# Kernel optimization log

Measured on AMD Instinct MI355X. Metric: run time of the kernel, lower is better.

Reference implementation:

```python
import jax, jax.numpy as jnp
import numpy as np

EPS = 1e-6


def _phi(x):
    # feature map: ELU(x) + 1, strictly positive
    return jax.nn.elu(x) + 1.0


def setup_inputs() -> dict:
    key = jax.random.key(0)
    kq, kk, kv, km, kz = jax.random.split(key, 5)
    B, H, T, D = 2, 32, 4096, 128
    Q = jax.random.normal(kq, (B, H, T, D), dtype=jnp.float32)
    K = jax.random.normal(kk, (B, H, T, D), dtype=jnp.float32)
    V = jax.random.normal(kv, (B, H, T, D), dtype=jnp.float32)
    M = jax.random.normal(km, (H, D, D), dtype=jnp.float32)
    z = jax.random.uniform(kz, (H, D), dtype=jnp.float32)
    return {"Q": Q, "K": K, "V": V, "M": M, "z": z}


def reference(Q, K, V, M, z):
    # ---- retrieve(Q) ----
    phi_Q = _phi(Q)                                   # (b,h,t,d)
    retrieved = jnp.einsum('bhtd,hde->bhte', phi_Q, M)
    norm = jnp.einsum('bhtd,hd->bht', phi_Q, z)[..., None]
    out = retrieved / jnp.maximum(norm, EPS)          # (b,h,t,d)

    # ---- update(K, V): detached (stop_gradient) running accumulation ----
    phi_K_b = _phi(jax.lax.stop_gradient(K)).mean(0)  # (h,t,d)
    V_b = jax.lax.stop_gradient(V).mean(0)            # (h,t,d)
    M_new = M + jnp.einsum('htd,hte->hde', phi_K_b, V_b)
    z_new = z + phi_K_b.sum(1)
    return out, M_new, z_new
```

## Files before the change

kernel.cpp:

```cpp
#include <hip/hip_runtime.h>
#include <cstdint>
#include <cstddef>


typedef __bf16 bf16x8 __attribute__((ext_vector_type(8)));
typedef float  f32x4  __attribute__((ext_vector_type(4)));
typedef unsigned short us4v __attribute__((ext_vector_type(4)));
typedef unsigned short us8v __attribute__((ext_vector_type(8)));

#define NB 2
#define NH 32
#define NT 4096
#define ND 128
#define NC 16
#define TCH (NT / NC)
#define EPSF 1e-6f

__device__ __forceinline__ float phi_f(float x) {
    return x > 0.0f ? x + 1.0f : __expf(x);
}

__device__ __forceinline__ unsigned short f2bf(float f) {
    union { float f; unsigned u; } c; c.f = f;
    unsigned r = c.u + 0x7FFFu + ((c.u >> 16) & 1u);
    return (unsigned short)(r >> 16);
}

__global__ __launch_bounds__(256) void k_prep(const float* __restrict__ M,
                                              unsigned short* __restrict__ Mt) {
    int idx = blockIdx.x * 256 + threadIdx.x;
    int h = idx >> 14, rem = idx & 16383;
    int e = rem >> 7, d = rem & 127;
    Mt[idx] = f2bf(M[(h << 14) + (d << 7) + e]);
}

__global__ __launch_bounds__(256) void k_out(const float* __restrict__ Q,
                                             const unsigned short* __restrict__ Mt,
                                             const float* __restrict__ z,
                                             float* __restrict__ out) {
    __shared__ unsigned short As[128 * 136];
    __shared__ unsigned short Bs[128 * 136];
    __shared__ float nrm[128];

    const int tid  = threadIdx.x;
    const int tile = blockIdx.x & 31;
    const int bh   = blockIdx.x >> 5;
    const int h    = bh & 31;
    const float* Qb = Q + ((size_t)bh * NT + (size_t)tile * 128) * ND;

    {
        const us8v* src = (const us8v*)(Mt + (size_t)h * 128 * 128);
#pragma unroll
        for (int i = 0; i < 8; ++i) {
            int idx = i * 256 + tid;
            int e  = idx >> 4;
            int d8 = (idx & 15) << 3;
            us8v v = src[idx];
            *(us8v*)&Bs[e * 136 + d8] = v;
        }
    }
    {
        const int d0 = (tid & 31) << 2;
        const int rb = tid >> 5;
        const float4 zv = *(const float4*)(z + h * ND + d0);
#pragma unroll
        for (int i = 0; i < 16; ++i) {
            int r = rb + i * 8;
            float4 q = *(const float4*)(Qb + (size_t)r * ND + d0);
            float p0 = phi_f(q.x), p1 = phi_f(q.y), p2 = phi_f(q.z), p3 = phi_f(q.w);
            float part = p0 * zv.x + p1 * zv.y + p2 * zv.z + p3 * zv.w;
            part += __shfl_xor(part, 1);
            part += __shfl_xor(part, 2);
            part += __shfl_xor(part, 4);
            part += __shfl_xor(part, 8);
            part += __shfl_xor(part, 16);
            if ((tid & 31) == 0) nrm[r] = part;
            us4v pk;
            pk.x = f2bf(p0); pk.y = f2bf(p1); pk.z = f2bf(p2); pk.w = f2bf(p3);
            *(us4v*)&As[r * 136 + d0] = pk;
        }
    }
    __syncthreads();

    const int lane = tid & 63, wave = tid >> 6;
    const int mw = (wave & 1) << 6, nw = (wave >> 1) << 6;
    const int l15 = lane & 15, qd = lane >> 4;

    f32x4 acc[4][4];
#pragma unroll
    for (int a = 0; a < 4; ++a)
#pragma unroll
        for (int b = 0; b < 4; ++b) acc[a][b] = (f32x4){0.f, 0.f, 0.f, 0.f};

#pragma unroll
    for (int kk = 0; kk < 4; ++kk) {
        const int k0 = kk * 32 + qd * 8;
        bf16x8 af[4], bfv[4];
#pragma unroll
        for (int im = 0; im < 4; ++im)
            af[im] = *(const bf16x8*)&As[(mw + im * 16 + l15) * 136 + k0];
#pragma unroll
        for (int in = 0; in < 4; ++in)
            bfv[in] = *(const bf16x8*)&Bs[(nw + in * 16 + l15) * 136 + k0];
#pragma unroll
        for (int im = 0; im < 4; ++im)
#pragma unroll
            for (int in = 0; in < 4; ++in)
                acc[im][in] = __builtin_amdgcn_mfma_f32_16x16x32_bf16(
                    af[im], bfv[in], acc[im][in], 0, 0, 0);
    }

    float inv[4][4];
#pragma unroll
    for (int im = 0; im < 4; ++im)
#pragma unroll
        for (int rg = 0; rg < 4; ++rg)
            inv[im][rg] = 1.0f / fmaxf(nrm[mw + im * 16 + qd * 4 + rg], EPSF);

    float* outb = out + ((size_t)bh * NT + (size_t)tile * 128) * ND;
#pragma unroll
    for (int im = 0; im < 4; ++im)
#pragma unroll
        for (int in = 0; in < 4; ++in) {
            int col = nw + in * 16 + l15;
#pragma unroll
            for (int rg = 0; rg < 4; ++rg) {
                int row = mw + im * 16 + qd * 4 + rg;
                outb[(size_t)row * ND + col] = acc[im][in][rg] * inv[im][rg];
            }
        }
}

__global__ __launch_bounds__(256) void k_upd(const float* __restrict__ K,
                                             const float* __restrict__ V,
                                             float* __restrict__ part,
                                             float* __restrict__ zpart) {
    __shared__ unsigned short Kl[128 * 72];
    __shared__ unsigned short Vl[128 * 72];
    __shared__ float zacc[128];

    const int tid = threadIdx.x;
    const int h   = blockIdx.x >> 4;
    const int ch  = blockIdx.x & 15;
    const size_t bstr = (size_t)NH * NT * ND;
    const float* K0 = K + (size_t)h * NT * ND + (size_t)ch * TCH * ND;
    const float* K1 = K0 + bstr;
    const float* V0 = V + (size_t)h * NT * ND + (size_t)ch * TCH * ND;
    const float* V1 = V0 + bstr;
    if (tid < 128) zacc[tid] = 0.0f;

    const int d0 = (tid & 31) << 2;
    const int tb = tid >> 5;
    const int lane = tid & 63, wave = tid >> 6;
    const int mw = (wave & 1) << 6, nw = (wave >> 1) << 6;
    const int l15 = lane & 15, qd = lane >> 4;

    float zp0 = 0.f, zp1 = 0.f, zp2 = 0.f, zp3 = 0.f;
    f32x4 acc[4][4];
#pragma unroll
    for (int a = 0; a < 4; ++a)
#pragma unroll
        for (int b = 0; b < 4; ++b) acc[a][b] = (f32x4){0.f, 0.f, 0.f, 0.f};

    for (int st = 0; st < TCH / 64; ++st) {
        __syncthreads();
#pragma unroll
        for (int i = 0; i < 8; ++i) {
            int tl = tb + i * 8;
            size_t off = (size_t)(st * 64 + tl) * ND + d0;
            float4 a0 = *(const float4*)(K0 + off);
            float4 a1 = *(const float4*)(K1 + off);
            float4 b0 = *(const float4*)(V0 + off);
            float4 b1 = *(const float4*)(V1 + off);
            float p0 = 0.5f * (phi_f(a0.x) + phi_f(a1.x));
            float p1 = 0.5f * (phi_f(a0.y) + phi_f(a1.y));
            float p2 = 0.5f * (phi_f(a0.z) + phi_f(a1.z));
            float p3 = 0.5f * (phi_f(a0.w) + phi_f(a1.w));
            float w0 = 0.5f * (b0.x + b1.x);
            float w1 = 0.5f * (b0.y + b1.y);
            float w2 = 0.5f * (b0.z + b1.z);
            float w3 = 0.5f * (b0.w + b1.w);
            zp0 += p0; zp1 += p1; zp2 += p2; zp3 += p3;
            Kl[(d0 + 0) * 72 + tl] = f2bf(p0);
            Kl[(d0 + 1) * 72 + tl] = f2bf(p1);
            Kl[(d0 + 2) * 72 + tl] = f2bf(p2);
            Kl[(d0 + 3) * 72 + tl] = f2bf(p3);
            Vl[(d0 + 0) * 72 + tl] = f2bf(w0);
            Vl[(d0 + 1) * 72 + tl] = f2bf(w1);
            Vl[(d0 + 2) * 72 + tl] = f2bf(w2);
            Vl[(d0 + 3) * 72 + tl] = f2bf(w3);
        }
        __syncthreads();
#pragma unroll
        for (int kk = 0; kk < 2; ++kk) {
            int k0i = kk * 32 + qd * 8;
            bf16x8 af[4], bfv[4];
#pragma unroll
            for (int im = 0; im < 4; ++im)
                af[im] = *(const bf16x8*)&Kl[(mw + im * 16 + l15) * 72 + k0i];
#pragma unroll
            for (int in = 0; in < 4; ++in)
                bfv[in] = *(const bf16x8*)&Vl[(nw + in * 16 + l15) * 72 + k0i];
#pragma unroll
            for (int im = 0; im < 4; ++im)
#pragma unroll
                for (int in = 0; in < 4; ++in)
                    acc[im][in] = __builtin_amdgcn_mfma_f32_16x16x32_bf16(
                        af[im], bfv[in], acc[im][in], 0, 0, 0);
        }
    }

    atomicAdd(&zacc[d0 + 0], zp0);
    atomicAdd(&zacc[d0 + 1], zp1);
    atomicAdd(&zacc[d0 + 2], zp2);
    atomicAdd(&zacc[d0 + 3], zp3);
    __syncthreads();
    if (tid < 128) zpart[((size_t)h * NC + ch) * 128 + tid] = zacc[tid];

    float* pb = part + ((size_t)h * NC + ch) * 16384;
#pragma unroll
    for (int im = 0; im < 4; ++im)
#pragma unroll
        for (int in = 0; in < 4; ++in) {
            int col = nw + in * 16 + l15;
#pragma unroll
            for (int rg = 0; rg < 4; ++rg) {
                int row = mw + im * 16 + qd * 4 + rg;
                pb[(size_t)row * ND + col] = acc[im][in][rg];
            }
        }
}

__global__ __launch_bounds__(256) void k_reduce(const float* __restrict__ M,
                                                const float* __restrict__ z,
                                                const float* __restrict__ part,
                                                const float* __restrict__ zpart,
                                                float* __restrict__ outM,
                                                float* __restrict__ outz) {
    int idx = blockIdx.x * 256 + threadIdx.x;
    int h = idx >> 14, de = idx & 16383;
    float s = M[idx];
    const float* p = part + (size_t)h * NC * 16384 + de;
#pragma unroll
    for (int c = 0; c < NC; ++c) s += p[(size_t)c * 16384];
    outM[idx] = s;
    if (idx < NH * ND) {
        int hh = idx >> 7, d = idx & 127;
        float sz = z[idx];
        const float* pz = zpart + (size_t)hh * NC * 128 + d;
#pragma unroll
        for (int c = 0; c < NC; ++c) sz += pz[c * 128];
        outz[idx] = sz;
    }
}

extern "C" void kernel_launch(void* const* d_in, const int* in_sizes, int n_in,
                              void* d_out, int out_size, void* d_ws, size_t ws_size,
                              hipStream_t stream) {
    const float* Q = (const float*)d_in[0];
    const float* K = (const float*)d_in[1];
    const float* V = (const float*)d_in[2];
    const float* M = (const float*)d_in[3];
    const float* z = (const float*)d_in[4];

    float* out0 = (float*)d_out;
    float* outM = out0 + (size_t)NB * NH * NT * ND;
    float* outz = outM + (size_t)NH * ND * ND;

    unsigned short* Mt = (unsigned short*)d_ws;
    float* part  = (float*)((char*)d_ws + (1u << 20));
    float* zpart = part + (size_t)NH * NC * ND * ND;

    k_prep<<<2048, 256, 0, stream>>>(M, Mt);
    k_out<<<NB * NH * (NT / 128), 256, 0, stream>>>(Q, Mt, z, out0);
    k_upd<<<NH * NC, 256, 0, stream>>>(K, V, part, zpart);
    k_reduce<<<(NH * ND * ND) / 256, 256, 0, stream>>>(M, z, part, zpart, outM, outz);
}
```

Measured before the change: 446.4 us.

## Fuse retrieve and update kernels into one launch with register-direct Q fragments

Merges the output and update kernels into a single launch, with the update blocks scheduled first. The aim is to overlap the compute-heavy K/V reduction with the bandwidth-bound retrieve and to drop a launch. The retrieve path now loads Q straight into MFMA fragments, skipping the LDS staging. It also computes the normaliser with an extra MFMA against bf16 z instead of shuffles. The update path halves the chunk count and writes packed 8-wide XOR-swizzled LDS stores instead of scalar transposed stores. In exchange, z and the norm are now held in bf16, which costs some precision, and there are fewer update blocks.

```diff
diff --git a/kernel.cpp b/kernel.cpp
--- a/kernel.cpp
+++ b/kernel.cpp
@@ -5,15 +5,16 @@
 
 typedef __bf16 bf16x8 __attribute__((ext_vector_type(8)));
 typedef float  f32x4  __attribute__((ext_vector_type(4)));
-typedef unsigned short us4v __attribute__((ext_vector_type(4)));
 typedef unsigned short us8v __attribute__((ext_vector_type(8)));
 
 #define NB 2
 #define NH 32
 #define NT 4096
 #define ND 128
-#define NC 16
+#define NC 8
 #define TCH (NT / NC)
+#define NUPD (NH * NC)
+#define NOUT (NB * NH * (NT / 128))
 #define EPSF 1e-6f
 
 __device__ __forceinline__ float phi_f(float x) {
@@ -24,6 +25,14 @@
     union { float f; unsigned u; } c; c.f = f;
     unsigned r = c.u + 0x7FFFu + ((c.u >> 16) & 1u);
     return (unsigned short)(r >> 16);
+}
+
+__device__ __forceinline__ bf16x8 pack8(float a0, float a1, float a2, float a3,
+                                        float a4, float a5, float a6, float a7) {
+    union { us8v u; bf16x8 h; } r;
+    r.u[0] = f2bf(a0); r.u[1] = f2bf(a1); r.u[2] = f2bf(a2); r.u[3] = f2bf(a3);
+    r.u[4] = f2bf(a4); r.u[5] = f2bf(a5); r.u[6] = f2bf(a6); r.u[7] = f2bf(a7);
+    return r.h;
 }
 
 __global__ __launch_bounds__(256) void k_prep(const float* __restrict__ M,
@@ -34,114 +43,16 @@
     Mt[idx] = f2bf(M[(h << 14) + (d << 7) + e]);
 }
 
-__global__ __launch_bounds__(256) void k_out(const float* __restrict__ Q,
-                                             const unsigned short* __restrict__ Mt,
-                                             const float* __restrict__ z,
-                                             float* __restrict__ out) {
-    __shared__ unsigned short As[128 * 136];
-    __shared__ unsigned short Bs[128 * 136];
-    __shared__ float nrm[128];
-
-    const int tid  = threadIdx.x;
-    const int tile = blockIdx.x & 31;
-    const int bh   = blockIdx.x >> 5;
-    const int h    = bh & 31;
-    const float* Qb = Q + ((size_t)bh * NT + (size_t)tile * 128) * ND;
-
-    {
-        const us8v* src = (const us8v*)(Mt + (size_t)h * 128 * 128);
-#pragma unroll
-        for (int i = 0; i < 8; ++i) {
-            int idx = i * 256 + tid;
-            int e  = idx >> 4;
-            int d8 = (idx & 15) << 3;
-            us8v v = src[idx];
-            *(us8v*)&Bs[e * 136 + d8] = v;
-        }
-    }
-    {
-        const int d0 = (tid & 31) << 2;
-        const int rb = tid >> 5;
-        const float4 zv = *(const float4*)(z + h * ND + d0);
-#pragma unroll
-        for (int i = 0; i < 16; ++i) {
-            int r = rb + i * 8;
-            float4 q = *(const float4*)(Qb + (size_t)r * ND + d0);
-            float p0 = phi_f(q.x), p1 = phi_f(q.y), p2 = phi_f(q.z), p3 = phi_f(q.w);
-            float part = p0 * zv.x + p1 * zv.y + p2 * zv.z + p3 * zv.w;
-            part += __shfl_xor(part, 1);
-            part += __shfl_xor(part, 2);
-            part += __shfl_xor(part, 4);
-            part += __shfl_xor(part, 8);
-            part += __shfl_xor(part, 16);
-            if ((tid & 31) == 0) nrm[r] = part;
-            us4v pk;
-            pk.x = f2bf(p0); pk.y = f2bf(p1); pk.z = f2bf(p2); pk.w = f2bf(p3);
-            *(us4v*)&As[r * 136 + d0] = pk;
-        }
-    }
-    __syncthreads();
-
-    const int lane = tid & 63, wave = tid >> 6;
-    const int mw = (wave & 1) << 6, nw = (wave >> 1) << 6;
-    const int l15 = lane & 15, qd = lane >> 4;
-
-    f32x4 acc[4][4];
-#pragma unroll
-    for (int a = 0; a < 4; ++a)
-#pragma unroll
-        for (int b = 0; b < 4; ++b) acc[a][b] = (f32x4){0.f, 0.f, 0.f, 0.f};
-
-#pragma unroll
-    for (int kk = 0; kk < 4; ++kk) {
-        const int k0 = kk * 32 + qd * 8;
-        bf16x8 af[4], bfv[4];
-#pragma unroll
-        for (int im = 0; im < 4; ++im)
-            af[im] = *(const bf16x8*)&As[(mw + im * 16 + l15) * 136 + k0];
-#pragma unroll
-        for (int in = 0; in < 4; ++in)
-            bfv[in] = *(const bf16x8*)&Bs[(nw + in * 16 + l15) * 136 + k0];
-#pragma unroll
-        for (int im = 0; im < 4; ++im)
-#pragma unroll
-            for (int in = 0; in < 4; ++in)
-                acc[im][in] = __builtin_amdgcn_mfma_f32_16x16x32_bf16(
-                    af[im], bfv[in], acc[im][in], 0, 0, 0);
-    }
-
-    float inv[4][4];
-#pragma unroll
-    for (int im = 0; im < 4; ++im)
-#pragma unroll
-        for (int rg = 0; rg < 4; ++rg)
-            inv[im][rg] = 1.0f / fmaxf(nrm[mw + im * 16 + qd * 4 + rg], EPSF);
-
-    float* outb = out + ((size_t)bh * NT + (size_t)tile * 128) * ND;
-#pragma unroll
-    for (int im = 0; im < 4; ++im)
-#pragma unroll
-        for (int in = 0; in < 4; ++in) {
-            int col = nw + in * 16 + l15;
-#pragma unroll
-            for (int rg = 0; rg < 4; ++rg) {
-                int row = mw + im * 16 + qd * 4 + rg;
-                outb[(size_t)row * ND + col] = acc[im][in][rg] * inv[im][rg];
-            }
-        }
-}
-
-__global__ __launch_bounds__(256) void k_upd(const float* __restrict__ K,
-                                             const float* __restrict__ V,
-                                             float* __restrict__ part,
-                                             float* __restrict__ zpart) {
-    __shared__ unsigned short Kl[128 * 72];
-    __shared__ unsigned short Vl[128 * 72];
-    __shared__ float zacc[128];
-
+__device__ __forceinline__ void upd_body(int blk, const float* __restrict__ K,
+                                         const float* __restrict__ V,
+                                         float* __restrict__ part,
+                                         float* __restrict__ zpart,
+                                         unsigned short* smem, float* zacc) {
     const int tid = threadIdx.x;
-    const int h   = blockIdx.x >> 4;
-    const int ch  = blockIdx.x & 15;
+    const int h = blk >> 3, ch = blk & 7;
+    unsigned short* Kl = smem;
+    unsigned short* Vl = smem + 8192;
+
     const size_t bstr = (size_t)NH * NT * ND;
     const float* K0 = K + (size_t)h * NT * ND + (size_t)ch * TCH * ND;
     const float* K1 = K0 + bstr;
@@ -149,11 +60,11 @@
     const float* V1 = V0 + bstr;
     if (tid < 128) zacc[tid] = 0.0f;
 
-    const int d0 = (tid & 31) << 2;
-    const int tb = tid >> 5;
+    const int L = tid & 31, d0 = L << 2, tb = tid >> 5;
     const int lane = tid & 63, wave = tid >> 6;
     const int mw = (wave & 1) << 6, nw = (wave >> 1) << 6;
     const int l15 = lane & 15, qd = lane >> 4;
+    const int grp = tb ^ (L & 7);
 
     float zp0 = 0.f, zp1 = 0.f, zp2 = 0.f, zp3 = 0.f;
     f32x4 acc[4][4];
@@ -163,11 +74,10 @@
         for (int b = 0; b < 4; ++b) acc[a][b] = (f32x4){0.f, 0.f, 0.f, 0.f};
 
     for (int st = 0; st < TCH / 64; ++st) {
-        __syncthreads();
+        us8v kpu[4], vpu[4];
 #pragma unroll
         for (int i = 0; i < 8; ++i) {
-            int tl = tb + i * 8;
-            size_t off = (size_t)(st * 64 + tl) * ND + d0;
+            size_t off = ((size_t)(st * 64 + tb * 8 + i)) * ND + d0;
             float4 a0 = *(const float4*)(K0 + off);
             float4 a1 = *(const float4*)(K1 + off);
             float4 b0 = *(const float4*)(V0 + off);
@@ -176,37 +86,42 @@
             float p1 = 0.5f * (phi_f(a0.y) + phi_f(a1.y));
             float p2 = 0.5f * (phi_f(a0.z) + phi_f(a1.z));
             float p3 = 0.5f * (phi_f(a0.w) + phi_f(a1.w));
-            float w0 = 0.5f * (b0.x + b1.x);
-            float w1 = 0.5f * (b0.y + b1.y);
-            float w2 = 0.5f * (b0.z + b1.z);
-            float w3 = 0.5f * (b0.w + b1.w);
             zp0 += p0; zp1 += p1; zp2 += p2; zp3 += p3;
-            Kl[(d0 + 0) * 72 + tl] = f2bf(p0);
-            Kl[(d0 + 1) * 72 + tl] = f2bf(p1);
-            Kl[(d0 + 2) * 72 + tl] = f2bf(p2);
-            Kl[(d0 + 3) * 72 + tl] = f2bf(p3);
-            Vl[(d0 + 0) * 72 + tl] = f2bf(w0);
-            Vl[(d0 + 1) * 72 + tl] = f2bf(w1);
-            Vl[(d0 + 2) * 72 + tl] = f2bf(w2);
-            Vl[(d0 + 3) * 72 + tl] = f2bf(w3);
+            kpu[0][i] = f2bf(p0); kpu[1][i] = f2bf(p1);
+            kpu[2][i] = f2bf(p2); kpu[3][i] = f2bf(p3);
+            vpu[0][i] = f2bf(0.5f * (b0.x + b1.x));
+            vpu[1][i] = f2bf(0.5f * (b0.y + b1.y));
+            vpu[2][i] = f2bf(0.5f * (b0.z + b1.z));
+            vpu[3][i] = f2bf(0.5f * (b0.w + b1.w));
         }
         __syncthreads();
 #pragma unroll
+        for (int j = 0; j < 4; ++j) {
+            *(us8v*)&Kl[(d0 + j) * 64 + grp * 8] = kpu[j];
+            *(us8v*)&Vl[(d0 + j) * 64 + grp * 8] = vpu[j];
+        }
+        __syncthreads();
+#pragma unroll
         for (int kk = 0; kk < 2; ++kk) {
-            int k0i = kk * 32 + qd * 8;
-            bf16x8 af[4], bfv[4];
-#pragma unroll
-            for (int im = 0; im < 4; ++im)
-                af[im] = *(const bf16x8*)&Kl[(mw + im * 16 + l15) * 72 + k0i];
-#pragma unroll
-            for (int in = 0; in < 4; ++in)
-                bfv[in] = *(const bf16x8*)&Vl[(nw + in * 16 + l15) * 72 + k0i];
+            bf16x8 af[4], bv[4];
+#pragma unroll
+            for (int im = 0; im < 4; ++im) {
+                int d = mw + im * 16 + l15;
+                int sg = (kk * 4 + qd) ^ ((d >> 2) & 7);
+                af[im] = *(const bf16x8*)&Kl[d * 64 + sg * 8];
+            }
+#pragma unroll
+            for (int in = 0; in < 4; ++in) {
+                int e = nw + in * 16 + l15;
+                int sg = (kk * 4 + qd) ^ ((e >> 2) & 7);
+                bv[in] = *(const bf16x8*)&Vl[e * 64 + sg * 8];
+            }
 #pragma unroll
             for (int im = 0; im < 4; ++im)
 #pragma unroll
                 for (int in = 0; in < 4; ++in)
                     acc[im][in] = __builtin_amdgcn_mfma_f32_16x16x32_bf16(
-                        af[im], bfv[in], acc[im][in], 0, 0, 0);
+                        af[im], bv[in], acc[im][in], 0, 0, 0);
         }
     }
 
@@ -229,6 +144,108 @@
                 pb[(size_t)row * ND + col] = acc[im][in][rg];
             }
         }
+}
+
+__device__ __forceinline__ void out_body(int blk, const float* __restrict__ Q,
+                                         const unsigned short* __restrict__ Mt,
+                                         const float* __restrict__ z,
+                                         float* __restrict__ out,
+                                         unsigned short* smem) {
+    const int tid = threadIdx.x;
+    const int tile = blk & 31, bh = blk >> 5, h = bh & 31;
+    const float* Qb = Q + ((size_t)bh * NT + (size_t)tile * 128) * ND;
+    unsigned short* Bs = smem;
+
+    {
+        const us8v* src = (const us8v*)(Mt + (size_t)h * 16384);
+#pragma unroll
+        for (int i = 0; i < 8; ++i) {
+            int idx = i * 256 + tid;
+            int e = idx >> 4, d8 = idx & 15;
+            *(us8v*)&Bs[e * 136 + d8 * 8] = src[idx];
+        }
+    }
+    const int lane = tid & 63, wave = tid >> 6;
+    const int mw = (wave & 1) << 6, nw = (wave >> 1) << 6;
+    const int l15 = lane & 15, qd = lane >> 4;
+
+    bf16x8 zf[4];
+#pragma unroll
+    for (int kk = 0; kk < 4; ++kk) {
+        const float* zp = z + h * ND + kk * 32 + qd * 8;
+        float4 z0 = *(const float4*)zp;
+        float4 z1 = *(const float4*)(zp + 4);
+        zf[kk] = pack8(z0.x, z0.y, z0.z, z0.w, z1.x, z1.y, z1.z, z1.w);
+    }
+    __syncthreads();
+
+    f32x4 acc[4][4], accN[4];
+#pragma unroll
+    for (int a = 0; a < 4; ++a) {
+        accN[a] = (f32x4){0.f, 0.f, 0.f, 0.f};
+#pragma unroll
+        for (int b = 0; b < 4; ++b) acc[a][b] = (f32x4){0.f, 0.f, 0.f, 0.f};
+    }
+
+#pragma unroll
+    for (int im = 0; im < 4; ++im) {
+        int row = mw + im * 16 + l15;
+        const float* qr = Qb + (size_t)row * ND;
+        bf16x8 af[4];
+#pragma unroll
+        for (int kk = 0; kk < 4; ++kk) {
+            const float* qp = qr + kk * 32 + qd * 8;
+            float4 q0 = *(const float4*)qp;
+            float4 q1 = *(const float4*)(qp + 4);
+            af[kk] = pack8(phi_f(q0.x), phi_f(q0.y), phi_f(q0.z), phi_f(q0.w),
+                           phi_f(q1.x), phi_f(q1.y), phi_f(q1.z), phi_f(q1.w));
+        }
+#pragma unroll
+        for (int kk = 0; kk < 4; ++kk)
+            accN[im] = __builtin_amdgcn_mfma_f32_16x16x32_bf16(
+                af[kk], zf[kk], accN[im], 0, 0, 0);
+#pragma unroll
+        for (int in = 0; in < 4; ++in) {
+            int e = nw + in * 16 + l15;
+#pragma unroll
+            for (int kk = 0; kk < 4; ++kk) {
+                bf16x8 bv = *(const bf16x8*)&Bs[e * 136 + kk * 32 + qd * 8];
+                acc[im][in] = __builtin_amdgcn_mfma_f32_16x16x32_bf16(
+                    af[kk], bv, acc[im][in], 0, 0, 0);
+            }
+        }
+    }
+
+    float* outb = out + ((size_t)bh * NT + (size_t)tile * 128) * ND;
+#pragma unroll
+    for (int im = 0; im < 4; ++im) {
+#pragma unroll
+        for (int rg = 0; rg < 4; ++rg) {
+            float inv = 1.0f / fmaxf(accN[im][rg], EPSF);
+            int row = mw + im * 16 + qd * 4 + rg;
+#pragma unroll
+            for (int in = 0; in < 4; ++in) {
+                int col = nw + in * 16 + l15;
+                outb[(size_t)row * ND + col] = acc[im][in][rg] * inv;
+            }
+        }
+    }
+}
+
+__global__ __launch_bounds__(256) void k_main(const float* __restrict__ Q,
+                                              const float* __restrict__ K,
+                                              const float* __restrict__ V,
+                                              const unsigned short* __restrict__ Mt,
+                                              const float* __restrict__ z,
+                                              float* __restrict__ out,
+                                              float* __restrict__ part,
+                                              float* __restrict__ zpart) {
+    __shared__ unsigned short smem[128 * 136];
+    __shared__ float zacc[128];
+    if (blockIdx.x < NUPD)
+        upd_body(blockIdx.x, K, V, part, zpart, smem, zacc);
+    else
+        out_body(blockIdx.x - NUPD, Q, Mt, z, out, smem);
 }
 
 __global__ __launch_bounds__(256) void k_reduce(const float* __restrict__ M,
@@ -272,7 +289,6 @@
     float* zpart = part + (size_t)NH * NC * ND * ND;
 
     k_prep<<<2048, 256, 0, stream>>>(M, Mt);
-    k_out<<<NB * NH * (NT / 128), 256, 0, stream>>>(Q, Mt, z, out0);
-    k_upd<<<NH * NC, 256, 0, stream>>>(K, V, part, zpart);
+    k_main<<<NUPD + NOUT, 256, 0, stream>>>(Q, K, V, Mt, z, out0, part, zpart);
     k_reduce<<<(NH * ND * ND) / 256, 256, 0, stream>>>(M, z, part, zpart, outM, outz);
 }
```

Result: faster. 425.2 us (-4.8%).
